# Kernel optimization log

Measured on AMD Instinct MI355X. Metric: run time of the kernel, lower is better.

Reference implementation:

```python
import jax, jax.numpy as jnp
import numpy as np

NUM_HEADS = 16
NUM_LANDMARKS = 64
N_ITER = 6


def iterative_inv(mat):
    # mat: (B, H, L, L) row-stochastic kernel; Newton-Schulz-style iteration
    L = mat.shape[-1]
    I = jnp.eye(L, dtype=mat.dtype)
    K = mat
    # init: V = K^T / max_j(sum_i K_ij)
    denom = jnp.max(jnp.sum(K, axis=-2), axis=-1)[:, :, None, None]
    Vm = (1.0 / denom) * jnp.swapaxes(K, -1, -2)
    for _ in range(N_ITER):
        KV = jnp.matmul(K, Vm)
        Vm = jnp.matmul(0.25 * Vm, 13.0 * I - jnp.matmul(KV, 15.0 * I - jnp.matmul(KV, 7.0 * I - KV)))
    return Vm


def setup_inputs() -> dict:
    key = jax.random.key(0)
    kq, kk, kv = jax.random.split(key, 3)
    B, N, C = 4, 4096, 1024
    return {
        "Q": jax.random.normal(kq, (B, N, C), dtype=jnp.float32),
        "K": jax.random.normal(kk, (B, N, C), dtype=jnp.float32),
        "V": jax.random.normal(kv, (B, N, C), dtype=jnp.float32),
    }


def reference(Q, K, V):
    B, N, C = Q.shape
    H, Lm = NUM_HEADS, NUM_LANDMARKS
    hd = C // H
    scale = hd ** 0.5
    # (B, H, N, hd)
    q = Q.reshape(B, N, H, hd).transpose(0, 2, 1, 3) / scale
    k = K.reshape(B, N, H, hd).transpose(0, 2, 1, 3)
    v = V.reshape(B, N, H, hd).transpose(0, 2, 1, 3)

    # landmark pooling (N divisible by Lm): mean over segments of length N//Lm
    seg = N // Lm
    k_lm = k.reshape(B, H, Lm, seg, hd).mean(axis=-2)  # (B,H,Lm,hd)
    q_lm = q.reshape(B, H, Lm, seg, hd).mean(axis=-2)  # (B,H,Lm,hd)

    kernel_1 = jax.nn.softmax(jnp.einsum('bhnd,bhld->bhnl', q, k_lm), axis=-1)   # (B,H,N,Lm)
    kernel_2 = jax.nn.softmax(jnp.einsum('bhmd,bhld->bhml', q_lm, k_lm), axis=-1)  # (B,H,Lm,Lm)
    kernel_3 = jax.nn.softmax(jnp.einsum('bhld,bhnd->bhln', q_lm, k), axis=-1)   # (B,H,Lm,N)

    out = jnp.matmul(jnp.matmul(kernel_1, iterative_inv(kernel_2)), jnp.matmul(kernel_3, v))
    return out.transpose(0, 2, 1, 3).reshape(B, N, C)
```

## Files before the change

### kernel.cpp

```cpp
#include <hip/hip_runtime.h>
#include <math.h>

#define BB 4
#define NN 4096
#define CC 1024
#define HH 16
#define HD 64
#define LM 64
#define SEG 64
#define BHN (BB*HH)
#define MATP 68
#define MATE (64*MATP)

typedef __attribute__((ext_vector_type(8))) short bf16x8;
typedef __attribute__((ext_vector_type(4))) short s16x4;
typedef __attribute__((ext_vector_type(4))) float f32x4;

__device__ __forceinline__ float shfl_sum16(float v) {
  v += __shfl_xor(v, 1, 16);
  v += __shfl_xor(v, 2, 16);
  v += __shfl_xor(v, 4, 16);
  v += __shfl_xor(v, 8, 16);
  return v;
}

__device__ __forceinline__ void split8(const float* f, bf16x8& hi, bf16x8& lo) {
#pragma unroll
  for (int i = 0; i < 8; ++i) {
    unsigned u = __builtin_bit_cast(unsigned, f[i]);
    float hf = __builtin_bit_cast(float, u & 0xFFFF0000u);
    hi[i] = (short)(u >> 16);
    float l = f[i] - hf;
    unsigned ul = __builtin_bit_cast(unsigned, l);
    lo[i] = (short)(ul >> 16);
  }
}

__device__ __forceinline__ void split4(const float* f, s16x4& hi, s16x4& lo) {
#pragma unroll
  for (int i = 0; i < 4; ++i) {
    unsigned u = __builtin_bit_cast(unsigned, f[i]);
    float hf = __builtin_bit_cast(float, u & 0xFFFF0000u);
    hi[i] = (short)(u >> 16);
    float l = f[i] - hf;
    unsigned ul = __builtin_bit_cast(unsigned, l);
    lo[i] = (short)(ul >> 16);
  }
}

__device__ __forceinline__ int planeAddr(int row, int cd) {
  int B = (row << 7) + (cd << 4);
  return B ^ ((row & 7) << 4);
}
__device__ __forceinline__ bf16x8 ldP(const short* __restrict__ P, int row, int cd) {
  return *(const bf16x8*)((const char*)P + planeAddr(row, cd));
}

__device__ __forceinline__ void xpose4(float x[4], int lane) {
  bool p1 = (lane >> 4) & 1;
  float s0 = p1 ? x[0] : x[1], s1 = p1 ? x[2] : x[3];
  float r0 = __shfl_xor(s0, 16, 64), r1 = __shfl_xor(s1, 16, 64);
  if (p1) { x[0] = r0; x[2] = r1; } else { x[1] = r0; x[3] = r1; }
  bool p2 = (lane >> 5) & 1;
  s0 = p2 ? x[0] : x[2]; s1 = p2 ? x[1] : x[3];
  r0 = __shfl_xor(s0, 32, 64); r1 = __shfl_xor(s1, 32, 64);
  if (p2) { x[0] = r0; x[1] = r1; } else { x[2] = r0; x[3] = r1; }
}

__global__ __launch_bounds__(256) void lm_kernel(
    const float* __restrict__ Q, const float* __restrict__ K,
    float* __restrict__ qlm, float* __restrict__ klm) {
  int bh = blockIdx.y; int b = bh >> 4; int h = bh & 15;
  int tid = threadIdx.x;
  int l = blockIdx.x * 4 + (tid >> 6);
  int d = tid & 63;
  const float* qbase = Q + ((size_t)b*NN + (size_t)l*SEG)*CC + h*HD + d;
  const float* kbase = K + ((size_t)b*NN + (size_t)l*SEG)*CC + h*HD + d;
  float sq = 0.f, sk = 0.f;
#pragma unroll 8
  for (int s = 0; s < SEG; ++s) {
    sq += qbase[(size_t)s*CC];
    sk += kbase[(size_t)s*CC];
  }
  qlm[(size_t)bh*4096 + l*64 + d] = sq * (1.0f/(64.0f*8.0f));
  klm[(size_t)bh*4096 + l*64 + d] = sk * (1.0f/64.0f);
}

__global__ __launch_bounds__(256, 3) void k3v_kernel(
    const float* __restrict__ K, const float* __restrict__ V,
    const float* __restrict__ qlm,
    float* __restrict__ S3, float* __restrict__ ACC3) {
  __shared__ alignas(16) short KEh[64*64], KEl[64*64];
  __shared__ alignas(16) short VtH[64*64], VtL[64*64];
  __shared__ alignas(16) float Erow[64*MATP];
  const int bh = blockIdx.y, b = bh >> 4, h = bh & 15;
  const int tile = blockIdx.x, tid = threadIdx.x;
  const int wid = tid >> 6, lane = tid & 63;
  const int lr = lane & 15, lg = lane >> 4;
  const int m0 = wid*16 + lg*4;

  bf16x8 qh[2], ql[2];
#pragma unroll
  for (int ks = 0; ks < 2; ++ks) {
    const float* qp = qlm + (size_t)bh*4096 + (wid*16 + lr)*64 + ks*32 + lg*8;
    float qf[8];
    *(float4*)&qf[0] = *(const float4*)qp;
    *(float4*)&qf[4] = *(const float4*)(qp + 4);
    split8(qf, qh[ks], ql[ks]);
  }

  f32x4 acc2[4];
#pragma unroll
  for (int t = 0; t < 4; ++t) acc2[t] = (f32x4){0.f, 0.f, 0.f, 0.f};
  float srow[4] = {0.f, 0.f, 0.f, 0.f};

  const int rk0 = tid >> 3,        ck = tid & 7;
  const int rk1 = (tid + 256) >> 3;
  const int dV  = 4*lr + lg;

  float4 gk[2][2], gv[4];

#define K3V_LOAD(SUB)                                                          \
  {                                                                            \
    const int n0_ = tile*128 + (SUB)*64;                                       \
    const float* kb0 = &K[((size_t)b*NN + n0_ + rk0)*CC + h*HD + ck*8];        \
    const float* kb1 = &K[((size_t)b*NN + n0_ + rk1)*CC + h*HD + ck*8];        \
    gk[0][0] = *(const float4*)kb0;  gk[0][1] = *(const float4*)(kb0 + 4);     \
    gk[1][0] = *(const float4*)kb1;  gk[1][1] = *(const float4*)(kb1 + 4);     \
    _Pragma("unroll")                                                          \
    for (int q = 0; q < 4; ++q) {                                              \
      int f = tid + 256*q;                                                     \
      int r = f >> 4, c4 = (f & 15) << 2;                                      \
      gv[q] = *(const float4*)&V[((size_t)b*NN + n0_ + r)*CC + h*HD + c4];     \
    }                                                                          \
  }

#define K3V_WRITE()                                                            \
  {                                                                            \
    _Pragma("unroll")                                                          \
    for (int q2 = 0; q2 < 2; ++q2) {                                           \
      float kf[8];                                                             \
      *(float4*)&kf[0] = gk[q2][0];                                            \
      *(float4*)&kf[4] = gk[q2][1];                                            \
      bf16x8 khv, klv; split8(kf, khv, klv);                                   \
      int r = q2 ? rk1 : rk0;                                                  \
      int A = planeAddr(r, ck);                                                \
      *(bf16x8*)((char*)KEh + A) = khv;                                        \
      *(bf16x8*)((char*)KEl + A) = klv;                                        \
    }                                                                          \
    _Pragma("unroll")                                                          \
    for (int q = 0; q < 4; ++q) {                                              \
      float x[4] = {gv[q].x, gv[q].y, gv[q].z, gv[q].w};                       \
      xpose4(x, lane);                                                         \
      int nb = 16*q + 4*wid;                                                   \
      s16x4 vh, vl; split4(x, vh, vl);                                         \
      int B = (dV << 7) + (nb << 1);                                           \
      B ^= (dV & 7) << 4;                                                      \
      *(s16x4*)((char*)VtH + B) = vh;                                          \
      *(s16x4*)((char*)VtL + B) = vl;                                          \
    }                                                                          \
  }

#define K3V_COMPUTE()                                                          \
  {                                                                            \
    f32x4 zacc[4];                                                             \
    _Pragma("unroll")                                                          \
    for (int t = 0; t < 4; ++t) zacc[t] = (f32x4){0.f, 0.f, 0.f, 0.f};        \
    _Pragma("unroll")                                                          \
    for (int ks = 0; ks < 2; ++ks) {                                           \
      _Pragma("unroll")                                                        \
      for (int tn = 0; tn < 4; ++tn) {                                         \
        bf16x8 bh_ = ldP(KEh, tn*16 + lr, 4*ks + lg);                          \
        bf16x8 bl_ = ldP(KEl, tn*16 + lr, 4*ks + lg);                          \
        zacc[tn] = __builtin_amdgcn_mfma_f32_16x16x32_bf16(qh[ks], bh_, zacc[tn], 0, 0, 0); \
        zacc[tn] = __builtin_amdgcn_mfma_f32_16x16x32_bf16(qh[ks], bl_, zacc[tn], 0, 0, 0); \
        zacc[tn] = __builtin_amdgcn_mfma_f32_16x16x32_bf16(ql[ks], bh_, zacc[tn], 0, 0, 0); \
      }                                                                        \
    }                                                                          \
    float e[4][4];                                                             \
    _Pragma("unroll")                                                          \
    for (int tn = 0; tn < 4; ++tn)                                             \
      _Pragma("unroll")                                                        \
      for (int r = 0; r < 4; ++r) e[tn][r] = __expf(zacc[tn][r]);              \
    _Pragma("unroll")                                                          \
    for (int r = 0; r < 4; ++r) {                                              \
      float t = e[0][r] + e[1][r] + e[2][r] + e[3][r];                         \
      srow[r] += shfl_sum16(t);                                                \
    }                                                                          \
    _Pragma("unroll")                                                          \
    for (int tn = 0; tn < 4; ++tn) {                                           \
      const int n = tn*16 + lr;                                                \
      _Pragma("unroll")                                                        \
      for (int r = 0; r < 4; ++r) Erow[(m0 + r)*MATP + n] = e[tn][r];          \
    }                                                                          \
    _Pragma("unroll")                                                          \
    for (int ks = 0; ks < 2; ++ks) {                                           \
      float fa[8];                                                             \
      const float* ap = Erow + (wid*16 + lr)*MATP + ks*32 + lg*8;              \
      *(float4*)&fa[0] = *(const float4*)ap;                                   \
      *(float4*)&fa[4] = *(const float4*)(ap + 4);                             \
      bf16x8 ah, al; split8(fa, ah, al);                                       \
      _Pragma("unroll")                                                        \
      for (int tn = 0; tn < 4; ++tn) {                                         \
        bf16x8 bh_ = ldP(VtH, tn*16 + lr, 4*ks + lg);                          \
        bf16x8 bl_ = ldP(VtL, tn*16 + lr, 4*ks + lg);                          \
        acc2[tn] = __builtin_amdgcn_mfma_f32_16x16x32_bf16(ah, bh_, acc2[tn], 0, 0, 0); \
        acc2[tn] = __builtin_amdgcn_mfma_f32_16x16x32_bf16(ah, bl_, acc2[tn], 0, 0, 0); \
        acc2[tn] = __builtin_amdgcn_mfma_f32_16x16x32_bf16(al, bh_, acc2[tn], 0, 0, 0); \
      }                                                                        \
    }                                                                          \
  }

  K3V_LOAD(0)
  K3V_WRITE()
  __syncthreads();
  K3V_LOAD(1)
  K3V_COMPUTE()
  __syncthreads();
  K3V_WRITE()
  __syncthreads();
  K3V_COMPUTE()

  if (lr == 0) {
#pragma unroll
    for (int r = 0; r < 4; ++r)
      atomicAdd(&S3[bh*64 + m0 + r], srow[r]);
  }
#pragma unroll
  for (int tn = 0; tn < 4; ++tn)
#pragma unroll
    for (int r = 0; r < 4; ++r)
      atomicAdd(&ACC3[(size_t)bh*4096 + (m0 + r)*64 + tn*16 + lr], acc2[tn][r]);
}

template<bool FUSE, bool HR, bool HC, bool HG>
__device__ __forceinline__ void mm_mfma(
    const float* __restrict__ Arow, const float* __restrict__ Scol,
    float diagc, float scale,
    float* __restrict__ OutRow, float* __restrict__ OutCol, float* __restrict__ OutGlob,
    int wid, int lane) {
  const int lr = lane & 15, lg = lane >> 4;
  f32x4 acc[4];
#pragma unroll
  for (int t = 0; t < 4; ++t) acc[t] = (f32x4){0.f, 0.f, 0.f, 0.f};

#pragma unroll
  for (int ks = 0; ks < 2; ++ks) {
    const int kb = ks*32 + lg*8;
    float fa[8];
    const float* ap = Arow + (wid*16 + lr)*MATP + kb;
#pragma unroll
    for (int i = 0; i < 4; ++i) { float2 t = *(const float2*)(ap + 2*i); fa[2*i] = t.x; fa[2*i+1] = t.y; }
    bf16x8 ah, al; split8(fa, ah, al);
#pragma unroll
    for (int tn = 0; tn < 4; ++tn) {
      float fb[8];
      const float* bp = Scol + (tn*16 + lr)*MATP + kb;
#pragma unroll
      for (int i = 0; i < 4; ++i) { float2 t = *(const float2*)(bp + 2*i); fb[2*i] = t.x; fb[2*i+1] = t.y; }
      if (FUSE) {
        int diff = (tn*16 + lr) - kb;
#pragma unroll
        for (int i = 0; i < 8; ++i) fb[i] = (i == diff ? diagc : 0.f) - fb[i];
      }
      bf16x8 bh_, bl_; split8(fb, bh_, bl_);
      acc[tn] = __builtin_amdgcn_mfma_f32_16x16x32_bf16(ah, bh_, acc[tn], 0, 0, 0);
      acc[tn] = __builtin_amdgcn_mfma_f32_16x16x32_bf16(ah, bl_, acc[tn], 0, 0, 0);
      acc[tn] = __builtin_amdgcn_mfma_f32_16x16x32_bf16(al, bh_, acc[tn], 0, 0, 0);
    }
  }
  __syncthreads();
#pragma unroll
  for (int tn = 0; tn < 4; ++tn) {
    float v0 = scale*acc[tn][0], v1 = scale*acc[tn][1], v2 = scale*acc[tn][2], v3 = scale*acc[tn][3];
    const int n = tn*16 + lr, m0 = wid*16 + lg*4;
    if (HC) *(float4*)&OutCol[n*MATP + m0] = make_float4(v0, v1, v2, v3);
    if (HR) {
      OutRow[(m0+0)*MATP + n] = v0;
      OutRow[(m0+1)*MATP + n] = v1;
      OutRow[(m0+2)*MATP + n] = v2;
      OutRow[(m0+3)*MATP + n] = v3;
    }
    if (HG) {
      OutGlob[(m0+0)*64 + n] = v0;
      OutGlob[(m0+1)*64 + n] = v1;
      OutGlob[(m0+2)*64 + n] = v2;
      OutGlob[(m0+3)*64 + n] = v3;
    }
  }
  __syncthreads();
}

__global__ __launch_bounds__(256) void inv_kernel(
    const float* __restrict__ qlm, const float* __restrict__ klm,
    const float* __restrict__ S3, const float* __restrict__ ACC3,
    float* __restrict__ W) {
  extern __shared__ float sm[];
  float* K2row = sm;
  float* Vmrow = sm + 1*MATE;
  float* Vmcol = sm + 2*MATE;
  float* Xrow  = sm + 3*MATE;
  float* Xcol  = sm + 4*MATE;
  float* Ycol  = sm + 5*MATE;
  float* Zcol  = sm + 6*MATE;
  float* red   = sm + 7*MATE;
  const int bh = blockIdx.x, tid = threadIdx.x;
  const int wid = tid >> 6, lane = tid & 63;
  const int lr = lane & 15, lg = lane >> 4;

#pragma unroll
  for (int q = 0; q < 4; ++q) {
    int f = tid + 256*q;
    int r = f >> 4, c4 = (f & 15) << 2;
    *(float4*)&Xrow[r*MATP + c4] = *(const float4*)&qlm[(size_t)bh*4096 + f*4];
    *(float4*)&Xcol[r*MATP + c4] = *(const float4*)&klm[(size_t)bh*4096 + f*4];
  }
  __syncthreads();

  {
    f32x4 zacc[4];
#pragma unroll
    for (int t = 0; t < 4; ++t) zacc[t] = (f32x4){0.f, 0.f, 0.f, 0.f};
#pragma unroll
    for (int ks = 0; ks < 2; ++ks) {
      const int kb = ks*32 + lg*8;
      float fa[8];
      const float* ap = Xrow + (wid*16 + lr)*MATP + kb;
#pragma unroll
      for (int i = 0; i < 4; ++i) { float2 t = *(const float2*)(ap + 2*i); fa[2*i] = t.x; fa[2*i+1] = t.y; }
      bf16x8 ah, al; split8(fa, ah, al);
#pragma unroll
      for (int tn = 0; tn < 4; ++tn) {
        float fb[8];
        const float* bp = Xcol + (tn*16 + lr)*MATP + kb;
#pragma unroll
        for (int i = 0; i < 4; ++i) { float2 t = *(const float2*)(bp + 2*i); fb[2*i] = t.x; fb[2*i+1] = t.y; }
        bf16x8 bh_, bl_; split8(fb, bh_, bl_);
        zacc[tn] = __builtin_amdgcn_mfma_f32_16x16x32_bf16(ah, bh_, zacc[tn], 0, 0, 0);
        zacc[tn] = __builtin_amdgcn_mfma_f32_16x16x32_bf16(ah, bl_, zacc[tn], 0, 0, 0);
        zacc[tn] = __builtin_amdgcn_mfma_f32_16x16x32_bf16(al, bh_, zacc[tn], 0, 0, 0);
      }
    }
    __syncthreads();
    float e[4][4];
#pragma unroll
    for (int tn = 0; tn < 4; ++tn)
#pragma unroll
      for (int r = 0; r < 4; ++r) e[tn][r] = __expf(zacc[tn][r]);
#pragma unroll
    for (int r = 0; r < 4; ++r) {
      float t = e[0][r] + e[1][r] + e[2][r] + e[3][r];
      t = shfl_sum16(t);
      float ri = 1.0f / t;
#pragma unroll
      for (int tn = 0; tn < 4; ++tn) e[tn][r] *= ri;
    }
    const int m0 = wid*16 + lg*4;
#pragma unroll
    for (int tn = 0; tn < 4; ++tn) {
      const int n = tn*16 + lr;
#pragma unroll
      for (int r = 0; r < 4; ++r) K2row[(m0+r)*MATP + n] = e[tn][r];
    }
  }
  __syncthreads();

  if (tid < 64) {
    float c = 0.f;
#pragma unroll 8
    for (int i = 0; i < 64; ++i) c += K2row[i*MATP + tid];
#pragma unroll
    for (int m = 1; m < 64; m <<= 1) c = fmaxf(c, __shfl_xor(c, m, 64));
    if (tid == 0) red[0] = 1.0f / c;
  }
  __syncthreads();
  const float invden = red[0];

#pragma unroll
  for (int q = 0; q < 4; ++q) {
    int f = tid + 256*q;
    int i = f >> 4, c4 = (f & 15) << 2;
    float4 kv = *(const float4*)&K2row[i*MATP + c4];
    kv.x *= invden; kv.y *= invden; kv.z *= invden; kv.w *= invden;
    *(float4*)&Vmcol[i*MATP + c4] = kv;
    Vmrow[(c4+0)*MATP + i] = kv.x;
    Vmrow[(c4+1)*MATP + i] = kv.y;
    Vmrow[(c4+2)*MATP + i] = kv.z;
    Vmrow[(c4+3)*MATP + i] = kv.w;
  }
  __syncthreads();

  for (int it = 0; it < 6; ++it) {
    mm_mfma<false, true,  true,  false>(K2row, Vmcol, 0.f,  1.0f,  Xrow, Xcol, nullptr, wid, lane);
    mm_mfma<true,  false, true,  false>(Xrow,  Xcol,  7.f,  1.0f,  nullptr, Ycol, nullptr, wid, lane);
    mm_mfma<true,  false, true,  false>(Xrow,  Ycol,  15.f, 1.0f,  nullptr, Zcol, nullptr, wid, lane);
    mm_mfma<true,  true,  true,  false>(Vmrow, Zcol,  13.f, 0.25f, Vmrow, Vmcol, nullptr, wid, lane);
  }

#pragma unroll
  for (int q = 0; q < 4; ++q) {
    int f = tid + 256*q;
    int k = f >> 4, c4 = (f & 15) << 2;
    float4 tv = *(const float4*)&ACC3[(size_t)bh*4096 + f*4];
    float ri = 1.0f / S3[bh*64 + k];
    Ycol[(c4+0)*MATP + k] = tv.x * ri;
    Ycol[(c4+1)*MATP + k] = tv.y * ri;
    Ycol[(c4+2)*MATP + k] = tv.z * ri;
    Ycol[(c4+3)*MATP + k] = tv.w * ri;
  }
  __syncthreads();
  mm_mfma<false, false, false, true>(Vmrow, Ycol, 0.f, 1.0f, nullptr, nullptr, W + (size_t)bh*4096, wid, lane);
}

__global__ __launch_bounds__(256, 3) void out_kernel(
    const float* __restrict__ Q, const float* __restrict__ klm,
    const float* __restrict__ W, float* __restrict__ Out) {
  __shared__ alignas(16) short KlH[64*64], KlL[64*64];
  __shared__ alignas(16) short WtH[64*64], WtL[64*64];
  __shared__ alignas(16) float Prow[64*MATP];
  const int bh = blockIdx.y, b = bh >> 4, h = bh & 15;
  const int n0 = blockIdx.x * 64;
  const int tid = threadIdx.x;
  const int wid = tid >> 6, lane = tid & 63;
  const int lr = lane & 15, lg = lane >> 4;
  const int m0 = wid*16 + lg*4;

#pragma unroll
  for (int q2 = 0; q2 < 2; ++q2) {
    int f = tid + 256*q2;
    int r = f >> 3, c = f & 7;
    const float* kp = &klm[(size_t)bh*4096 + r*64 + c*8];
    float kf[8];
    *(float4*)&kf[0] = *(const float4*)kp;
    *(float4*)&kf[4] = *(const float4*)(kp + 4);
    bf16x8 khv, klv; split8(kf, khv, klv);
    int A = planeAddr(r, c);
    *(bf16x8*)((char*)KlH + A) = khv;
    *(bf16x8*)((char*)KlL + A) = klv;
  }
  const int dW = 4*lr + lg;
#pragma unroll
  for (int q = 0; q < 4; ++q) {
    int f = tid + 256*q;
    int r = f >> 4, c4 = (f & 15) << 2;
    float4 wv = *(const float4*)&W[(size_t)bh*4096 + r*64 + c4];
    float x[4] = {wv.x, wv.y, wv.z, wv.w};
    xpose4(x, lane);
    int nb = 16*q + 4*wid;
    s16x4 wh, wl; split4(x, wh, wl);
    int B = (dW << 7) + (nb << 1);
    B ^= (dW & 7) << 4;
    *(s16x4*)((char*)WtH + B) = wh;
    *(s16x4*)((char*)WtL + B) = wl;
  }

  bf16x8 qh[2], qlo[2];
#pragma unroll
  for (int ks = 0; ks < 2; ++ks) {
    const float* qp = Q + ((size_t)b*NN + n0 + wid*16 + lr)*CC + h*HD + ks*32 + lg*8;
    float qf[8];
    *(float4*)&qf[0] = *(const float4*)qp;
    *(float4*)&qf[4] = *(const float4*)(qp + 4);
#pragma unroll
    for (int i = 0; i < 8; ++i) qf[i] *= 0.125f;
    split8(qf, qh[ks], qlo[ks]);
  }
  __syncthreads();

  f32x4 zacc[4];
#pragma unroll
  for (int t = 0; t < 4; ++t) zacc[t] = (f32x4){0.f, 0.f, 0.f, 0.f};
#pragma unroll
  for (int ks = 0; ks < 2; ++ks) {
#pragma unroll
    for (int tn = 0; tn < 4; ++tn) {
      bf16x8 bh_ = ldP(KlH, tn*16 + lr, 4*ks + lg);
      bf16x8 bl_ = ldP(KlL, tn*16 + lr, 4*ks + lg);
      zacc[tn] = __builtin_amdgcn_mfma_f32_16x16x32_bf16(qh[ks], bh_, zacc[tn], 0, 0, 0);
      zacc[tn] = __builtin_amdgcn_mfma_f32_16x16x32_bf16(qh[ks], bl_, zacc[tn], 0, 0, 0);
      zacc[tn] = __builtin_amdgcn_mfma_f32_16x16x32_bf16(qlo[ks], bh_, zacc[tn], 0, 0, 0);
    }
  }
  float e[4][4];
#pragma unroll
  for (int tn = 0; tn < 4; ++tn)
#pragma unroll
    for (int r = 0; r < 4; ++r) e[tn][r] = __expf(zacc[tn][r]);
#pragma unroll
  for (int r = 0; r < 4; ++r) {
    float t = e[0][r] + e[1][r] + e[2][r] + e[3][r];
    t = shfl_sum16(t);
    float ri = 1.0f / t;
#pragma unroll
    for (int tn = 0; tn < 4; ++tn) e[tn][r] *= ri;
  }
#pragma unroll
  for (int tn = 0; tn < 4; ++tn) {
    const int n = tn*16 + lr;
#pragma unroll
    for (int r = 0; r < 4; ++r) Prow[(m0+r)*MATP + n] = e[tn][r];
  }

  f32x4 oacc[4];
#pragma unroll
  for (int t = 0; t < 4; ++t) oacc[t] = (f32x4){0.f, 0.f, 0.f, 0.f};
#pragma unroll
  for (int ks = 0; ks < 2; ++ks) {
    float fa[8];
    const float* ap = Prow + (wid*16 + lr)*MATP + ks*32 + lg*8;
    *(float4*)&fa[0] = *(const float4*)ap;
    *(float4*)&fa[4] = *(const float4*)(ap + 4);
    bf16x8 ah, al; split8(fa, ah, al);
#pragma unroll
    for (int tn = 0; tn < 4; ++tn) {
      bf16x8 bh_ = ldP(WtH, tn*16 + lr, 4*ks + lg);
      bf16x8 bl_ = ldP(WtL, tn*16 + lr, 4*ks + lg);
      oacc[tn] = __builtin_amdgcn_mfma_f32_16x16x32_bf16(ah, bh_, oacc[tn], 0, 0, 0);
      oacc[tn] = __builtin_amdgcn_mfma_f32_16x16x32_bf16(ah, bl_, oacc[tn], 0, 0, 0);
      oacc[tn] = __builtin_amdgcn_mfma_f32_16x16x32_bf16(al, bh_, oacc[tn], 0, 0, 0);
    }
  }
#pragma unroll
  for (int tn = 0; tn < 4; ++tn) {
    const int d = tn*16 + lr;
#pragma unroll
    for (int r = 0; r < 4; ++r)
      Out[((size_t)b*NN + n0 + m0 + r)*CC + h*HD + d] = oacc[tn][r];
  }
}

extern "C" void kernel_launch(void* const* d_in, const int* in_sizes, int n_in,
                              void* d_out, int out_size, void* d_ws, size_t ws_size,
                              hipStream_t stream) {
  const float* Q = (const float*)d_in[0];
  const float* K = (const float*)d_in[1];
  const float* V = (const float*)d_in[2];
  float* out = (float*)d_out;
  float* ws  = (float*)d_ws;

  float* qlm  = ws;
  float* klm  = ws + 262144;
  float* S3   = ws + 524288;
  float* ACC3 = ws + 528384;
  float* Wm   = ws + 790528;

  size_t shC = (size_t)(7*MATE + 4)*sizeof(float);
  hipFuncSetAttribute((const void*)inv_kernel,
                      hipFuncAttributeMaxDynamicSharedMemorySize, (int)shC);

  hipMemsetAsync(S3, 0, (4096 + 262144)*sizeof(float), stream);

  lm_kernel <<<dim3(16, BHN), 256, 0, stream>>>(Q, K, qlm, klm);
  k3v_kernel<<<dim3(32, BHN), 256, 0, stream>>>(K, V, qlm, S3, ACC3);
  inv_kernel<<<dim3(BHN),     256, shC, stream>>>(qlm, klm, S3, ACC3, Wm);
  out_kernel<<<dim3(64, BHN), 256, 0, stream>>>(Q, klm, Wm, out);
}
```

Baseline: 147.7 us.

## Widen inverse kernel to 16 waves, one MFMA output tile per wave

The iterative-inverse kernel now runs 1024 threads per block instead of 256. Each of the 16 waves computes a single 16x16 output tile of every 64x64 matmul, where before each wave looped over four column tiles. The row-softmax normalisation of kernel_2 becomes a cross-wave reduction through a small shared buffer. Only 64 blocks exist, so this targets the latency of the serial Newton-Schulz chain, at the cost of more barrier participants and less per-wave instruction-level parallelism.

```diff
diff --git a/kernel.cpp b/kernel.cpp
--- a/kernel.cpp
+++ b/kernel.cpp
@@ -238,60 +238,52 @@
     const float* __restrict__ Arow, const float* __restrict__ Scol,
     float diagc, float scale,
     float* __restrict__ OutRow, float* __restrict__ OutCol, float* __restrict__ OutGlob,
-    int wid, int lane) {
+    int wr, int tn, int lane) {
   const int lr = lane & 15, lg = lane >> 4;
-  f32x4 acc[4];
-#pragma unroll
-  for (int t = 0; t < 4; ++t) acc[t] = (f32x4){0.f, 0.f, 0.f, 0.f};
+  f32x4 acc = (f32x4){0.f, 0.f, 0.f, 0.f};
 
 #pragma unroll
   for (int ks = 0; ks < 2; ++ks) {
     const int kb = ks*32 + lg*8;
     float fa[8];
-    const float* ap = Arow + (wid*16 + lr)*MATP + kb;
-#pragma unroll
-    for (int i = 0; i < 4; ++i) { float2 t = *(const float2*)(ap + 2*i); fa[2*i] = t.x; fa[2*i+1] = t.y; }
+    const float* ap = Arow + (wr*16 + lr)*MATP + kb;
+    *(float4*)&fa[0] = *(const float4*)ap;
+    *(float4*)&fa[4] = *(const float4*)(ap + 4);
     bf16x8 ah, al; split8(fa, ah, al);
-#pragma unroll
-    for (int tn = 0; tn < 4; ++tn) {
-      float fb[8];
-      const float* bp = Scol + (tn*16 + lr)*MATP + kb;
-#pragma unroll
-      for (int i = 0; i < 4; ++i) { float2 t = *(const float2*)(bp + 2*i); fb[2*i] = t.x; fb[2*i+1] = t.y; }
-      if (FUSE) {
-        int diff = (tn*16 + lr) - kb;
-#pragma unroll
-        for (int i = 0; i < 8; ++i) fb[i] = (i == diff ? diagc : 0.f) - fb[i];
-      }
-      bf16x8 bh_, bl_; split8(fb, bh_, bl_);
-      acc[tn] = __builtin_amdgcn_mfma_f32_16x16x32_bf16(ah, bh_, acc[tn], 0, 0, 0);
-      acc[tn] = __builtin_amdgcn_mfma_f32_16x16x32_bf16(ah, bl_, acc[tn], 0, 0, 0);
-      acc[tn] = __builtin_amdgcn_mfma_f32_16x16x32_bf16(al, bh_, acc[tn], 0, 0, 0);
+    float fb[8];
+    const float* bp = Scol + (tn*16 + lr)*MATP + kb;
+    *(float4*)&fb[0] = *(const float4*)bp;
+    *(float4*)&fb[4] = *(const float4*)(bp + 4);
+    if (FUSE) {
+      int diff = (tn*16 + lr) - kb;
+#pragma unroll
+      for (int i = 0; i < 8; ++i) fb[i] = (i == diff ? diagc : 0.f) - fb[i];
     }
-  }
-  __syncthreads();
-#pragma unroll
-  for (int tn = 0; tn < 4; ++tn) {
-    float v0 = scale*acc[tn][0], v1 = scale*acc[tn][1], v2 = scale*acc[tn][2], v3 = scale*acc[tn][3];
-    const int n = tn*16 + lr, m0 = wid*16 + lg*4;
-    if (HC) *(float4*)&OutCol[n*MATP + m0] = make_float4(v0, v1, v2, v3);
-    if (HR) {
-      OutRow[(m0+0)*MATP + n] = v0;
-      OutRow[(m0+1)*MATP + n] = v1;
-      OutRow[(m0+2)*MATP + n] = v2;
-      OutRow[(m0+3)*MATP + n] = v3;
-    }
-    if (HG) {
-      OutGlob[(m0+0)*64 + n] = v0;
-      OutGlob[(m0+1)*64 + n] = v1;
-      OutGlob[(m0+2)*64 + n] = v2;
-      OutGlob[(m0+3)*64 + n] = v3;
-    }
-  }
-  __syncthreads();
-}
-
-__global__ __launch_bounds__(256) void inv_kernel(
+    bf16x8 bh_, bl_; split8(fb, bh_, bl_);
+    acc = __builtin_amdgcn_mfma_f32_16x16x32_bf16(ah, bh_, acc, 0, 0, 0);
+    acc = __builtin_amdgcn_mfma_f32_16x16x32_bf16(ah, bl_, acc, 0, 0, 0);
+    acc = __builtin_amdgcn_mfma_f32_16x16x32_bf16(al, bh_, acc, 0, 0, 0);
+  }
+  __syncthreads();
+  const int n = tn*16 + lr, m0 = wr*16 + lg*4;
+  float v0 = scale*acc[0], v1 = scale*acc[1], v2 = scale*acc[2], v3 = scale*acc[3];
+  if (HC) *(float4*)&OutCol[n*MATP + m0] = make_float4(v0, v1, v2, v3);
+  if (HR) {
+    OutRow[(m0+0)*MATP + n] = v0;
+    OutRow[(m0+1)*MATP + n] = v1;
+    OutRow[(m0+2)*MATP + n] = v2;
+    OutRow[(m0+3)*MATP + n] = v3;
+  }
+  if (HG) {
+    OutGlob[(m0+0)*64 + n] = v0;
+    OutGlob[(m0+1)*64 + n] = v1;
+    OutGlob[(m0+2)*64 + n] = v2;
+    OutGlob[(m0+3)*64 + n] = v3;
+  }
+  __syncthreads();
+}
+
+__global__ __launch_bounds__(1024, 1) void inv_kernel(
     const float* __restrict__ qlm, const float* __restrict__ klm,
     const float* __restrict__ S3, const float* __restrict__ ACC3,
     float* __restrict__ W) {
@@ -303,65 +295,58 @@
   float* Xcol  = sm + 4*MATE;
   float* Ycol  = sm + 5*MATE;
   float* Zcol  = sm + 6*MATE;
-  float* red   = sm + 7*MATE;
+  float* rs    = sm + 7*MATE;
+  float* rinv  = rs + 256;
+  float* red   = rinv + 64;
   const int bh = blockIdx.x, tid = threadIdx.x;
   const int wid = tid >> 6, lane = tid & 63;
+  const int wr = wid & 3, tn = wid >> 2;
   const int lr = lane & 15, lg = lane >> 4;
-
-#pragma unroll
-  for (int q = 0; q < 4; ++q) {
-    int f = tid + 256*q;
-    int r = f >> 4, c4 = (f & 15) << 2;
+  const int m0 = wr*16 + lg*4, n = tn*16 + lr;
+
+  {
+    int f = tid, r = f >> 4, c4 = (f & 15) << 2;
     *(float4*)&Xrow[r*MATP + c4] = *(const float4*)&qlm[(size_t)bh*4096 + f*4];
     *(float4*)&Xcol[r*MATP + c4] = *(const float4*)&klm[(size_t)bh*4096 + f*4];
   }
   __syncthreads();
 
   {
-    f32x4 zacc[4];
-#pragma unroll
-    for (int t = 0; t < 4; ++t) zacc[t] = (f32x4){0.f, 0.f, 0.f, 0.f};
+    f32x4 zacc = (f32x4){0.f, 0.f, 0.f, 0.f};
 #pragma unroll
     for (int ks = 0; ks < 2; ++ks) {
       const int kb = ks*32 + lg*8;
       float fa[8];
-      const float* ap = Xrow + (wid*16 + lr)*MATP + kb;
-#pragma unroll
-      for (int i = 0; i < 4; ++i) { float2 t = *(const float2*)(ap + 2*i); fa[2*i] = t.x; fa[2*i+1] = t.y; }
+      const float* ap = Xrow + (wr*16 + lr)*MATP + kb;
+      *(float4*)&fa[0] = *(const float4*)ap;
+      *(float4*)&fa[4] = *(const float4*)(ap + 4);
       bf16x8 ah, al; split8(fa, ah, al);
-#pragma unroll
-      for (int tn = 0; tn < 4; ++tn) {
-        float fb[8];
-        const float* bp = Xcol + (tn*16 + lr)*MATP + kb;
-#pragma unroll
-        for (int i = 0; i < 4; ++i) { float2 t = *(const float2*)(bp + 2*i); fb[2*i] = t.x; fb[2*i+1] = t.y; }
-        bf16x8 bh_, bl_; split8(fb, bh_, bl_);
-        zacc[tn] = __builtin_amdgcn_mfma_f32_16x16x32_bf16(ah, bh_, zacc[tn], 0, 0, 0);
-        zacc[tn] = __builtin_amdgcn_mfma_f32_16x16x32_bf16(ah, bl_, zacc[tn], 0, 0, 0);
-        zacc[tn] = __builtin_amdgcn_mfma_f32_16x16x32_bf16(al, bh_, zacc[tn], 0, 0, 0);
-      }
+      float fb[8];
+      const float* bp = Xcol + (tn*16 + lr)*MATP + kb;
+      *(float4*)&fb[0] = *(const float4*)bp;
+      *(float4*)&fb[4] = *(const float4*)(bp + 4);
+      bf16x8 bh_, bl_; split8(fb, bh_, bl_);
+      zacc = __builtin_amdgcn_mfma_f32_16x16x32_bf16(ah, bh_, zacc, 0, 0, 0);
+      zacc = __builtin_amdgcn_mfma_f32_16x16x32_bf16(ah, bl_, zacc, 0, 0, 0);
+      zacc = __builtin_amdgcn_mfma_f32_16x16x32_bf16(al, bh_, zacc, 0, 0, 0);
+    }
+    float e[4];
+#pragma unroll
+    for (int r = 0; r < 4; ++r) e[r] = __expf(zacc[r]);
+    float part[4];
+#pragma unroll
+    for (int r = 0; r < 4; ++r) part[r] = shfl_sum16(e[r]);
+    if (lr == 0) {
+#pragma unroll
+      for (int r = 0; r < 4; ++r) rs[(m0 + r)*4 + tn] = part[r];
     }
     __syncthreads();
-    float e[4][4];
-#pragma unroll
-    for (int tn = 0; tn < 4; ++tn)
-#pragma unroll
-      for (int r = 0; r < 4; ++r) e[tn][r] = __expf(zacc[tn][r]);
-#pragma unroll
-    for (int r = 0; r < 4; ++r) {
-      float t = e[0][r] + e[1][r] + e[2][r] + e[3][r];
-      t = shfl_sum16(t);
-      float ri = 1.0f / t;
-#pragma unroll
-      for (int tn = 0; tn < 4; ++tn) e[tn][r] *= ri;
-    }
-    const int m0 = wid*16 + lg*4;
-#pragma unroll
-    for (int tn = 0; tn < 4; ++tn) {
-      const int n = tn*16 + lr;
-#pragma unroll
-      for (int r = 0; r < 4; ++r) K2row[(m0+r)*MATP + n] = e[tn][r];
-    }
+    if (tid < 64)
+      rinv[tid] = 1.0f / (rs[tid*4] + rs[tid*4+1] + rs[tid*4+2] + rs[tid*4+3]);
+    __syncthreads();
+#pragma unroll
+    for (int r = 0; r < 4; ++r)
+      K2row[(m0+r)*MATP + n] = e[r] * rinv[m0 + r];
   }
   __syncthreads();
 
@@ -376,10 +361,8 @@
   __syncthreads();
   const float invden = red[0];
 
-#pragma unroll
-  for (int q = 0; q < 4; ++q) {
-    int f = tid + 256*q;
-    int i = f >> 4, c4 = (f & 15) << 2;
+  {
+    int f = tid, i = f >> 4, c4 = (f & 15) << 2;
     float4 kv = *(const float4*)&K2row[i*MATP + c4];
     kv.x *= invden; kv.y *= invden; kv.z *= invden; kv.w *= invden;
     *(float4*)&Vmcol[i*MATP + c4] = kv;
@@ -391,16 +374,14 @@
   __syncthreads();
 
   for (int it = 0; it < 6; ++it) {
-    mm_mfma<false, true,  true,  false>(K2row, Vmcol, 0.f,  1.0f,  Xrow, Xcol, nullptr, wid, lane);
-    mm_mfma<true,  false, true,  false>(Xrow,  Xcol,  7.f,  1.0f,  nullptr, Ycol, nullptr, wid, lane);
-    mm_mfma<true,  false, true,  false>(Xrow,  Ycol,  15.f, 1.0f,  nullptr, Zcol, nullptr, wid, lane);
-    mm_mfma<true,  true,  true,  false>(Vmrow, Zcol,  13.f, 0.25f, Vmrow, Vmcol, nullptr, wid, lane);
-  }
-
-#pragma unroll
-  for (int q = 0; q < 4; ++q) {
-    int f = tid + 256*q;
-    int k = f >> 4, c4 = (f & 15) << 2;
+    mm_mfma<false, true,  true,  false>(K2row, Vmcol, 0.f,  1.0f,  Xrow, Xcol, nullptr, wr, tn, lane);
+    mm_mfma<true,  false, true,  false>(Xrow,  Xcol,  7.f,  1.0f,  nullptr, Ycol, nullptr, wr, tn, lane);
+    mm_mfma<true,  false, true,  false>(Xrow,  Ycol,  15.f, 1.0f,  nullptr, Zcol, nullptr, wr, tn, lane);
+    mm_mfma<true,  true,  true,  false>(Vmrow, Zcol,  13.f, 0.25f, Vmrow, Vmcol, nullptr, wr, tn, lane);
+  }
+
+  {
+    int f = tid, k = f >> 4, c4 = (f & 15) << 2;
     float4 tv = *(const float4*)&ACC3[(size_t)bh*4096 + f*4];
     float ri = 1.0f / S3[bh*64 + k];
     Ycol[(c4+0)*MATP + k] = tv.x * ri;
@@ -409,7 +390,7 @@
     Ycol[(c4+3)*MATP + k] = tv.w * ri;
   }
   __syncthreads();
-  mm_mfma<false, false, false, true>(Vmrow, Ycol, 0.f, 1.0f, nullptr, nullptr, W + (size_t)bh*4096, wid, lane);
+  mm_mfma<false, false, false, true>(Vmrow, Ycol, 0.f, 1.0f, nullptr, nullptr, W + (size_t)bh*4096, wr, tn, lane);
 }
 
 __global__ __launch_bounds__(256, 3) void out_kernel(
@@ -544,7 +525,7 @@
   float* ACC3 = ws + 528384;
   float* Wm   = ws + 790528;
 
-  size_t shC = (size_t)(7*MATE + 4)*sizeof(float);
+  size_t shC = (size_t)(7*MATE + 384)*sizeof(float);
   hipFuncSetAttribute((const void*)inv_kernel,
                       hipFuncAttributeMaxDynamicSharedMemorySize, (int)shC);
 
@@ -552,6 +533,6 @@
 
   lm_kernel <<<dim3(16, BHN), 256, 0, stream>>>(Q, K, qlm, klm);
   k3v_kernel<<<dim3(32, BHN), 256, 0, stream>>>(K, V, qlm, S3, ACC3);
-  inv_kernel<<<dim3(BHN),     256, shC, stream>>>(qlm, klm, S3, ACC3, Wm);
+  inv_kernel<<<dim3(BHN),    1024, shC, stream>>>(qlm, klm, S3, ACC3, Wm);
   out_kernel<<<dim3(64, BHN), 256, 0, stream>>>(Q, klm, Wm, out);
 }
```

After: 141.0 us. 4.5% less time.
